# Performance work log

Measured on AMD Instinct MI355X. Metric: run time of the kernel, lower is better.

The kernel has to match this reference:

```python
import jax, jax.numpy as jnp
from jax import lax
import numpy as np

B, S, G = 16, 384, 384
N = S + G
E_CHAR, D = 100, 128
H = D // 2              # LSTM hidden per direction
NHEAD, NHID = 4, 64
T = 21                  # crf_input_dim = label_alphabet.size() + 1
START, STOP = T - 2, T - 1
ALPHA = 0.2
CHAR_V, GAZ_V = 8000, 100000
NEG = -9e15             # pyGAT masked_fill value


def setup_inputs():
    key = jax.random.key(0)
    ks = jax.random.split(key, 20)
    f32 = jnp.float32
    def nrm(k, shape, s=0.05):
        return (jax.random.normal(k, shape) * s).astype(f32)
    eye = jnp.eye(N, dtype=bool)
    def adj(k):
        return ((jax.random.uniform(k, (B, N, N)) < 0.1) | eye[None]).astype(jnp.int32)
    return dict(
        batch_char=jax.random.randint(ks[0], (B, S), 0, CHAR_V),
        batch_len=jnp.full((B,), S, jnp.int32),
        gaz_list=jax.random.randint(ks[1], (B, G), 0, GAZ_V),
        t_graph=adj(ks[2]), c_graph=adj(ks[3]), l_graph=adj(ks[4]),
        mask=jnp.ones((B, S), jnp.int32),
        char_table=nrm(ks[5], (CHAR_V, E_CHAR)),
        gaz_table=nrm(ks[6], (GAZ_V, D)),
        w_ih_f=nrm(ks[7], (4 * H, E_CHAR)), w_hh_f=nrm(ks[8], (4 * H, H)),
        b_f=jnp.zeros((4 * H,), f32),
        w_ih_b=nrm(ks[9], (4 * H, E_CHAR)), w_hh_b=nrm(ks[10], (4 * H, H)),
        b_b=jnp.zeros((4 * H,), f32),
        h2h_W=nrm(ks[11], (T, D)), h2h_b=jnp.zeros((T,), f32),
        gat_Wh=nrm(ks[12], (3, NHEAD, D, NHID)),
        gat_ah=nrm(ks[13], (3, NHEAD, 2 * NHID)),
        gat_Wo=nrm(ks[14], (3, NHEAD * NHID, T)),
        gat_ao=nrm(ks[15], (3, 2 * T)),
        fuse_w=jnp.ones((4,), f32),
        transitions=nrm(ks[16], (T, T)),
    )


def _lstm_dir(x, w_ih, w_hh, b, reverse):
    # x: [B,S,E]; torch gate order i,f,g,o
    Bb = x.shape[0]
    Hh = w_hh.shape[1]
    xw = jnp.einsum('bse,ge->bsg', x, w_ih) + b
    def step(carry, xt):
        h, c = carry
        g = xt + h @ w_hh.T
        i, f, gg, o = jnp.split(g, 4, axis=-1)
        c = jax.nn.sigmoid(f) * c + jax.nn.sigmoid(i) * jnp.tanh(gg)
        h = jax.nn.sigmoid(o) * jnp.tanh(c)
        return (h, c), h
    h0 = jnp.zeros((Bb, Hh), x.dtype)
    _, hs = lax.scan(step, (h0, h0), xw.swapaxes(0, 1), reverse=reverse)
    return hs.swapaxes(0, 1)


def _gat_layer(x, adj, W, a, concat):
    # pyGAT batched layer: e_ij = LeakyReLU(a . [Wh_i || Wh_j]), masked softmax over j
    h = jnp.einsum('bnd,df->bnf', x, W)
    F_ = W.shape[1]
    f1 = h @ a[:F_]           # [B,N]
    f2 = h @ a[F_:]
    e = jax.nn.leaky_relu(f1[:, :, None] + f2[:, None, :], negative_slope=ALPHA)
    e = jnp.where(adj > 0, e, NEG)
    att = jax.nn.softmax(e, axis=-1)
    out = jnp.einsum('bij,bjf->bif', att, h)
    return jax.nn.elu(out) if concat else out


def _gat(x, adj, Wh, ah, Wo, ao):
    heads = jax.vmap(lambda W, a: _gat_layer(x, adj, W, a, True))(Wh, ah)  # [H,B,N,F]
    hcat = jnp.moveaxis(heads, 0, 2).reshape(x.shape[0], x.shape[1], -1)
    return jax.nn.elu(_gat_layer(hcat, adj, Wo, ao, False))


def _crf_feature(batch_char, gaz_list, graphs, char_table, gaz_table,
                 w_ih_f, w_hh_f, b_f, w_ih_b, w_hh_b, b_b, h2h_W, h2h_b,
                 gat_Wh, gat_ah, gat_Wo, gat_ao, fuse_w):
    emb = char_table[batch_char]                      # [B,S,E_CHAR]
    hf = _lstm_dir(emb, w_ih_f, w_hh_f, b_f, False)
    hb = _lstm_dir(emb, w_ih_b, w_hh_b, b_b, True)
    lstm_feat = jnp.concatenate([hf, hb], axis=-1)    # [B,S,D]
    gaz_feat = gaz_table[gaz_list]                    # [B,G,D]
    gat_in = jnp.concatenate([lstm_feat, gaz_feat], axis=1)  # [B,N,D]
    gat_outs = [_gat(gat_in, adj, gat_Wh[k], gat_ah[k], gat_Wo[k], gat_ao[k])[:, :S]
                for k, adj in enumerate(graphs)]
    lstm_proj = lstm_feat @ h2h_W.T + h2h_b           # [B,S,T]
    return (fuse_w[0] * lstm_proj + fuse_w[1] * gat_outs[0]
            + fuse_w[2] * gat_outs[1] + fuse_w[3] * gat_outs[2])


def _viterbi(feats, transitions, mask):
    Bb, Ss, Tt = feats.shape
    ids = jnp.arange(Tt)
    part0 = feats[:, 0, :] + transitions[START][None, :]
    def step(part, inp):
        feat_t, m_t = inp
        cur = part[:, :, None] + transitions[None] + feat_t[:, None, :]  # [B,prev,cur]
        new = cur.max(axis=1)
        bp = cur.argmax(axis=1)
        m = (m_t > 0)[:, None]
        return jnp.where(m, new, part), jnp.where(m, bp, ids[None, :])
    part, bps = lax.scan(step, part0,
                         (feats[:, 1:].swapaxes(0, 1), mask[:, 1:].swapaxes(0, 1)))
    last_tag = jnp.argmax(part + transitions[:, STOP][None, :], axis=1)
    def back(tag, bp):
        prev = jnp.take_along_axis(bp, tag[:, None], axis=1)[:, 0]
        return prev, prev
    _, prevs = lax.scan(back, last_tag, bps, reverse=True)   # prevs[j] = tag at time j
    return jnp.concatenate([prevs.swapaxes(0, 1), last_tag[:, None]], axis=1)


def reference(batch_char, batch_len, gaz_list, t_graph, c_graph, l_graph, mask,
              char_table, gaz_table, w_ih_f, w_hh_f, b_f, w_ih_b, w_hh_b, b_b,
              h2h_W, h2h_b, gat_Wh, gat_ah, gat_Wo, gat_ao, fuse_w, transitions):
    # batch_len is all == S (mask all ones), so packed BiLSTM == plain BiLSTM
    feats = _crf_feature(batch_char, gaz_list, (t_graph, c_graph, l_graph),
                         char_table, gaz_table, w_ih_f, w_hh_f, b_f,
                         w_ih_b, w_hh_b, b_b, h2h_W, h2h_b,
                         gat_Wh, gat_ah, gat_Wo, gat_ao, fuse_w)
    return _viterbi(feats, transitions, mask)
```

## Files before the change

kernel.cpp:

```cpp
#include <hip/hip_runtime.h>
#include <hip/hip_bf16.h>
#include <cstdint>
#include <cstddef>

#define BB 16
#define SS 384
#define GG 384
#define NN 768
#define DD 128
#define EC 100
#define TT 21
#define NHEADS 4
#define BN (BB*NN)
#define BS (BB*SS)

#define GAZ_BASE  32
#define PACK_BASE (32 + 3072)
#define PRE_GRID  (PACK_BASE + 3 * BN)

#define H1SZ   3145728
#define OUT1SZ 3145728
#define H2SZ   258048
#define FGSZ   49152
#define FOSZ   12288
#define OUT2SZ 129024
#define PKSZ   ((size_t)BN * 12)

typedef float v2f __attribute__((ext_vector_type(2)));

__device__ __forceinline__ float sigf(float x) { return 1.0f / (1.0f + __expf(-x)); }
__device__ __forceinline__ float tanh_fast(float x) {
    return 1.0f - 2.0f / (__expf(2.0f * x) + 1.0f);
}
__device__ __forceinline__ float wred_max(float v) {
    #pragma unroll
    for (int o = 32; o > 0; o >>= 1) v = fmaxf(v, __shfl_xor(v, o));
    return v;
}
__device__ __forceinline__ float wred_sum(float v) {
    #pragma unroll
    for (int o = 32; o > 0; o >>= 1) v += __shfl_xor(v, o);
    return v;
}

__global__ __launch_bounds__(256) void k_xw(
    const int* __restrict__ batch_char, const float* __restrict__ char_table,
    const float* __restrict__ w_ih_f, const float* __restrict__ b_f,
    const float* __restrict__ w_ih_b, const float* __restrict__ b_b,
    float* __restrict__ xw_f, float* __restrict__ xw_b)
{
    __shared__ float At[EC * 68];
    __shared__ float Bt[EC * 68];
    __shared__ int   chs[64];
    const int tid = threadIdx.x;
    const int rt  = blockIdx.x;
    const int ot  = blockIdx.y;
    const int dir = ot >> 2, gt = ot & 3;
    const float* wih  = dir ? w_ih_b : w_ih_f;
    const float* bias = dir ? b_b    : b_f;
    float*       out  = dir ? xw_b   : xw_f;

    if (tid < 64) chs[tid] = batch_char[rt * 64 + tid];
    __syncthreads();
    for (int idx = tid; idx < 64 * EC; idx += 256) {
        int r = idx / EC, e = idx - r * EC;
        At[e * 68 + r] = char_table[(size_t)chs[r] * EC + e];
        Bt[e * 68 + r] = wih[(size_t)(gt * 64 + r) * EC + e];
    }
    __syncthreads();

    const int ty = tid >> 4, tx = tid & 15;
    const int r0 = ty * 4, c0 = tx * 4;
    float acc[4][4] = {};
    #pragma unroll 4
    for (int e = 0; e < EC; ++e) {
        float4 a = *(const float4*)&At[e * 68 + r0];
        float4 bv = *(const float4*)&Bt[e * 68 + c0];
        float av[4] = {a.x, a.y, a.z, a.w};
        float bb[4] = {bv.x, bv.y, bv.z, bv.w};
        #pragma unroll
        for (int i = 0; i < 4; ++i)
            #pragma unroll
            for (int j = 0; j < 4; ++j) acc[i][j] = fmaf(av[i], bb[j], acc[i][j]);
    }
    #pragma unroll
    for (int i = 0; i < 4; ++i) {
        int row = rt * 64 + r0 + i;
        int gc  = gt * 64 + c0;
        float4 o;
        o.x = acc[i][0] + bias[gc + 0];
        o.y = acc[i][1] + bias[gc + 1];
        o.z = acc[i][2] + bias[gc + 2];
        o.w = acc[i][3] + bias[gc + 3];
        *(float4*)&out[(size_t)row * 256 + gc] = o;
    }
}

__global__ __launch_bounds__(256) void k_pre(
    const float* __restrict__ xw_f, const float* __restrict__ xw_b,
    const float* __restrict__ w_hh_f, const float* __restrict__ w_hh_b,
    float* __restrict__ gat_in,
    const int* __restrict__ gaz_list, const float* __restrict__ gaz_table,
    const int* __restrict__ adj0, const int* __restrict__ adj1,
    const int* __restrict__ adj2, unsigned long long* __restrict__ packed)
{
    __shared__ float part[2][4][64][4];
    __shared__ float hbuf[4][64];
    const int bid = blockIdx.x;
    const int tid = threadIdx.x;

    if (bid < 32) {
        const int wv = tid >> 6, lane = tid & 63;
        const int b = bid >> 1, dir = bid & 1;
        const float* xw  = (dir ? xw_b : xw_f) + (size_t)b * SS * 256;
        const float* whh = dir ? w_hh_b : w_hh_f;
        v2f w2[4][8];
        #pragma unroll
        for (int g4 = 0; g4 < 4; ++g4) {
            const float* r = whh + (size_t)(g4 * 64 + lane) * 64 + 16 * wv;
            #pragma unroll
            for (int jj = 0; jj < 8; ++jj) w2[g4][jj] = v2f{r[2 * jj], r[2 * jj + 1]};
        }
        hbuf[wv][lane] = 0.f;
        float c = 0.f;
        int buf = 0;
        const int t0 = dir ? (SS - 1) : 0;
        float x0 = xw[t0 * 256 +   0 + lane];
        float x1 = xw[t0 * 256 +  64 + lane];
        float x2 = xw[t0 * 256 + 128 + lane];
        float x3 = xw[t0 * 256 + 192 + lane];
        const v2f* h2p = (const v2f*)&hbuf[wv][16 * wv];
        for (int tt = 0; tt < SS; ++tt) {
            const int t = dir ? (SS - 1 - tt) : tt;
            const int tn = dir ? (t - 1) : (t + 1);
            v2f a0 = v2f{0.f, 0.f}, a1 = v2f{0.f, 0.f}, a2 = v2f{0.f, 0.f}, a3 = v2f{0.f, 0.f};
            #pragma unroll
            for (int jj = 0; jj < 8; ++jj) {
                v2f hv = h2p[jj];
                a0 = __builtin_elementwise_fma(hv, w2[0][jj], a0);
                a1 = __builtin_elementwise_fma(hv, w2[1][jj], a1);
                a2 = __builtin_elementwise_fma(hv, w2[2][jj], a2);
                a3 = __builtin_elementwise_fma(hv, w2[3][jj], a3);
            }
            float4 pw;
            pw.x = a0.x + a0.y; pw.y = a1.x + a1.y;
            pw.z = a2.x + a2.y; pw.w = a3.x + a3.y;
            *(float4*)part[buf][wv][lane] = pw;
            float nx0 = 0.f, nx1 = 0.f, nx2 = 0.f, nx3 = 0.f;
            if (tt + 1 < SS) {
                nx0 = xw[tn * 256 +   0 + lane];
                nx1 = xw[tn * 256 +  64 + lane];
                nx2 = xw[tn * 256 + 128 + lane];
                nx3 = xw[tn * 256 + 192 + lane];
            }
            __syncthreads();
            float4 p0 = *(const float4*)part[buf][0][lane];
            float4 p1 = *(const float4*)part[buf][1][lane];
            float4 p2 = *(const float4*)part[buf][2][lane];
            float4 p3 = *(const float4*)part[buf][3][lane];
            float gi = ((p0.x + p1.x) + (p2.x + p3.x)) + x0;
            float gf = ((p0.y + p1.y) + (p2.y + p3.y)) + x1;
            float gg = ((p0.z + p1.z) + (p2.z + p3.z)) + x2;
            float go = ((p0.w + p1.w) + (p2.w + p3.w)) + x3;
            float nc = sigf(gf) * c + sigf(gi) * tanh_fast(gg);
            float nh = sigf(go) * tanh_fast(nc);
            c = nc;
            hbuf[wv][lane] = nh;
            if (wv == 0) gat_in[((size_t)b * NN + t) * DD + dir * 64 + lane] = nh;
            x0 = nx0; x1 = nx1; x2 = nx2; x3 = nx3;
            buf ^= 1;
        }
    } else if (bid < PACK_BASE) {
        int idx = (bid - GAZ_BASE) * 256 + tid;
        int d = idx & 127;
        int rest = idx >> 7;
        int g = rest % GG;
        int b = rest / GG;
        int gi = __builtin_nontemporal_load(&gaz_list[b * GG + g]);
        float v = __builtin_nontemporal_load(&gaz_table[(size_t)gi * DD + d]);
        gat_in[((size_t)b * NN + SS + g) * DD + d] = v;
    } else {
        const int row = bid - PACK_BASE;
        const int k = row / BN, n = row - k * BN;
        const int* adjk = (k == 0) ? adj0 : ((k == 1) ? adj1 : adj2);
        const int wave = tid >> 6, lane = tid & 63;
        #pragma unroll
        for (int it = 0; it < 3; ++it) {
            int j = it * 256 + tid;
            int a = __builtin_nontemporal_load(&adjk[(size_t)n * NN + j]);
            unsigned long long m = __ballot(a > 0);
            if (lane == 0)
                packed[((size_t)k * BN + n) * 12 + it * 4 + wave] = m;
        }
    }
}

__global__ __launch_bounds__(256) void k_p1(
    const float* __restrict__ gat_in, const float* __restrict__ gat_Wh,
    const float* __restrict__ gat_ah, int k0,
    float* __restrict__ h1, float* __restrict__ f1g, float* __restrict__ f2g,
    size_t zh1, size_t zfg)
{
    __shared__ float At[64 * 68];
    __shared__ float Bt[64 * 68];
    __shared__ float sf1[64], sf2[64];
    const int tid = threadIdx.x;
    const int rt = blockIdx.x, hd = blockIdx.y, z = blockIdx.z;
    const int k = k0 + z;
    float* h1p = h1 + (size_t)z * zh1;
    float* f1p = f1g + (size_t)z * zfg;
    float* f2p = f2g + (size_t)z * zfg;
    if (tid < 64) { sf1[tid] = 0.f; sf2[tid] = 0.f; }
    const float* W = gat_Wh + ((size_t)(k * NHEADS + hd)) * DD * 64;
    const int ty = tid >> 4, tx = tid & 15;
    const int r0 = ty * 4, c0 = tx * 4;
    float acc[4][4] = {};
    for (int ph = 0; ph < 2; ++ph) {
        __syncthreads();
        for (int idx = tid; idx < 64 * 64; idx += 256) {
            int r = idx >> 6, e = idx & 63;
            At[e * 68 + r] = gat_in[((size_t)(rt * 64 + r)) * DD + ph * 64 + e];
            int rB = idx & 63, eB = idx >> 6;
            Bt[eB * 68 + rB] = W[(size_t)(ph * 64 + eB) * 64 + rB];
        }
        __syncthreads();
        #pragma unroll 4
        for (int e = 0; e < 64; ++e) {
            float4 a = *(const float4*)&At[e * 68 + r0];
            float4 bv = *(const float4*)&Bt[e * 68 + c0];
            float av[4] = {a.x, a.y, a.z, a.w};
            float bb[4] = {bv.x, bv.y, bv.z, bv.w};
            #pragma unroll
            for (int i = 0; i < 4; ++i)
                #pragma unroll
                for (int j = 0; j < 4; ++j) acc[i][j] = fmaf(av[i], bb[j], acc[i][j]);
        }
    }
    const float* ah = gat_ah + (size_t)(k * NHEADS + hd) * 128;
    float a1[4], a2[4];
    #pragma unroll
    for (int j = 0; j < 4; ++j) { a1[j] = ah[c0 + j]; a2[j] = ah[64 + c0 + j]; }
    #pragma unroll
    for (int i = 0; i < 4; ++i) {
        int n = rt * 64 + r0 + i;
        float4 o = make_float4(acc[i][0], acc[i][1], acc[i][2], acc[i][3]);
        *(float4*)&h1p[((size_t)n * NHEADS + hd) * 64 + c0] = o;
        float p1 = acc[i][0] * a1[0] + acc[i][1] * a1[1] + acc[i][2] * a1[2] + acc[i][3] * a1[3];
        float p2 = acc[i][0] * a2[0] + acc[i][1] * a2[1] + acc[i][2] * a2[2] + acc[i][3] * a2[3];
        atomicAdd(&sf1[r0 + i], p1);
        atomicAdd(&sf2[r0 + i], p2);
    }
    __syncthreads();
    if (tid < 64) {
        f1p[hd * BN + rt * 64 + tid] = sf1[tid];
        f2p[hd * BN + rt * 64 + tid] = sf2[tid];
    }
}

__global__ __launch_bounds__(256) void k_attn1(
    const unsigned long long* __restrict__ packed, const float* __restrict__ h1,
    const float* __restrict__ f1g, const float* __restrict__ f2g,
    float* __restrict__ out1,
    size_t zpk, size_t zh1, size_t zfg, size_t zout1)
{
    __shared__ int   nbr[NN];
    __shared__ float ep[NHEADS][NN];
    __shared__ int cntS;
    const int tid = threadIdx.x, wave = tid >> 6, lane = tid & 63;
    const int bid = blockIdx.x, z = blockIdx.z;
    const int xcd = bid & 7;
    const int local = bid >> 3;
    const int b = 2 * xcd + ((local >= NN) ? 1 : 0);
    const int i = (local >= NN) ? (local - NN) : local;
    const int n = b * NN + i;
    const unsigned long long* pkp = packed + (size_t)z * zpk;
    const float* h1p = h1 + (size_t)z * zh1;
    const float* f1p = f1g + (size_t)z * zfg;
    const float* f2gp = f2g + (size_t)z * zfg;
    float* out1p = out1 + (size_t)z * zout1;
    if (wave == 0) {
        unsigned long long m = (lane < 12) ? pkp[(size_t)n * 12 + lane] : 0ULL;
        int pc = __popcll(m);
        int inc = pc;
        #pragma unroll
        for (int d = 1; d < 16; d <<= 1) { int t = __shfl_up(inc, d); if (lane >= d) inc += t; }
        int C = __shfl(inc, 11);
        if (lane == 0) cntS = C;
        int off = inc - pc;
        while (m) {
            int bit = __builtin_ctzll(m);
            nbr[off++] = lane * 64 + bit;
            m &= m - 1;
        }
    }
    __syncthreads();
    const int C = cntS;
    const int hd = wave;
    const float f1 = f1p[hd * BN + n];
    const float* f2p = f2gp + hd * BN + b * NN;
    float mx = -3.0e38f;
    for (int t = lane; t < C; t += 64) {
        float e = f1 + f2p[nbr[t]];
        e = (e >= 0.f) ? e : 0.2f * e;
        ep[hd][t] = e;
        mx = fmaxf(mx, e);
    }
    mx = wred_max(mx);
    float sum = 0.f;
    for (int t = lane; t < C; t += 64) {
        float p = __expf(ep[hd][t] - mx);
        ep[hd][t] = p;
        sum += p;
    }
    sum = wred_sum(sum);
    const float* hb = h1p + (size_t)b * NN * (NHEADS * 64) + hd * 64 + lane;
    float ac0 = 0.f, ac1 = 0.f, ac2 = 0.f, ac3 = 0.f;
    int t = 0;
    for (; t + 3 < C; t += 4) {
        int j0 = nbr[t], j1 = nbr[t + 1], j2 = nbr[t + 2], j3 = nbr[t + 3];
        float p0 = ep[hd][t], p1 = ep[hd][t + 1], p2 = ep[hd][t + 2], p3 = ep[hd][t + 3];
        ac0 = fmaf(p0, hb[(size_t)j0 * 256], ac0);
        ac1 = fmaf(p1, hb[(size_t)j1 * 256], ac1);
        ac2 = fmaf(p2, hb[(size_t)j2 * 256], ac2);
        ac3 = fmaf(p3, hb[(size_t)j3 * 256], ac3);
    }
    for (; t < C; ++t) ac0 = fmaf(ep[hd][t], hb[(size_t)nbr[t] * 256], ac0);
    float r = ((ac0 + ac1) + (ac2 + ac3)) / sum;
    r = (r > 0.f) ? r : expm1f(r);
    __builtin_nontemporal_store(r, &out1p[(size_t)n * 256 + hd * 64 + lane]);
}

__global__ __launch_bounds__(256) void k_p2(
    const float* __restrict__ out1, const float* __restrict__ gat_Wo,
    const float* __restrict__ gat_ao, int k0,
    float* __restrict__ h2, float* __restrict__ f1o, float* __restrict__ f2o,
    size_t zout1, size_t zh2, size_t zfo)
{
    __shared__ float ld[12 * 256];
    __shared__ float lf1[12], lf2[12];
    const int tid = threadIdx.x;
    const int blk = blockIdx.x, z = blockIdx.z;
    const int k = k0 + z;
    const float* out1p = out1 + (size_t)z * zout1;
    float* h2p = h2 + (size_t)z * zh2;
    float* f1op = f1o + (size_t)z * zfo;
    float* f2op = f2o + (size_t)z * zfo;
    if (tid < 12) { lf1[tid] = 0.f; lf2[tid] = 0.f; }
    for (int idx = tid; idx < 12 * 256; idx += 256)
        ld[idx] = out1p[(size_t)blk * 12 * 256 + idx];
    __syncthreads();
    if (tid < 252) {
        const int r = tid / TT, c = tid - r * TT;
        const float* Wo = gat_Wo + (size_t)k * 256 * TT;
        const float4* row4 = (const float4*)&ld[r * 256];
        float acc = 0.f;
        #pragma unroll 8
        for (int q4 = 0; q4 < 64; ++q4) {
            float4 v = row4[q4];
            int q = q4 * 4;
            acc = fmaf(v.x, Wo[(q + 0) * TT + c], acc);
            acc = fmaf(v.y, Wo[(q + 1) * TT + c], acc);
            acc = fmaf(v.z, Wo[(q + 2) * TT + c], acc);
            acc = fmaf(v.w, Wo[(q + 3) * TT + c], acc);
        }
        const int n = blk * 12 + r;
        h2p[(size_t)n * TT + c] = acc;
        const float* ao = gat_ao + k * 2 * TT;
        atomicAdd(&lf1[r], acc * ao[c]);
        atomicAdd(&lf2[r], acc * ao[TT + c]);
    }
    __syncthreads();
    if (tid < 12) {
        f1op[blk * 12 + tid] = lf1[tid];
        f2op[blk * 12 + tid] = lf2[tid];
    }
}

__global__ __launch_bounds__(64) void k_attn2(
    const unsigned long long* __restrict__ packed,
    const float* __restrict__ h2, const float* __restrict__ f1o,
    const float* __restrict__ f2o, float* __restrict__ out2,
    size_t zpk, size_t zh2, size_t zfo, size_t zout2)
{
    __shared__ int   nbr[NN];
    __shared__ float ep[NN];
    const int lane = threadIdx.x;
    const int bid = blockIdx.x, z = blockIdx.z;
    const int xcd = bid & 7;
    const int local = bid >> 3;
    const int b = 2 * xcd + ((local >= SS) ? 1 : 0);
    const int s = (local >= SS) ? (local - SS) : local;
    const int blk = b * SS + s;
    const int n = b * NN + s;
    const unsigned long long* pkp = packed + (size_t)z * zpk;
    const float* h2p = h2 + (size_t)z * zh2;
    const float* f1op = f1o + (size_t)z * zfo;
    const float* f2op = f2o + (size_t)z * zfo;
    float* out2k = out2 + (size_t)z * zout2;
    unsigned long long w64 = (lane < 12) ? pkp[(size_t)n * 12 + lane] : 0ULL;
    int pc = __popcll(w64);
    int inc = pc;
    #pragma unroll
    for (int d = 1; d < 16; d <<= 1) {
        int t = __shfl_up(inc, d, 16);
        if ((lane & 15) >= d) inc += t;
    }
    const int C = __shfl(inc, 11);
    int off = inc - pc;
    while (w64) {
        int bit = __builtin_ctzll(w64);
        nbr[off++] = lane * 64 + bit;
        w64 &= w64 - 1;
    }
    __syncthreads();
    const float f1 = f1op[n];
    const float* f2p = f2op + b * NN;
    float mx = -3.0e38f;
    for (int t = lane; t < C; t += 64) {
        int j = nbr[t];
        float e = f1 + f2p[j];
        e = (e >= 0.f) ? e : 0.2f * e;
        ep[t] = e;
        mx = fmaxf(mx, e);
    }
    mx = wred_max(mx);
    float sum = 0.f;
    for (int t = lane; t < C; t += 64) {
        float p = __expf(ep[t] - mx);
        ep[t] = p;
        sum += p;
    }
    sum = wred_sum(sum);
    const float* h2b = h2p + (size_t)b * NN * TT + ((lane < TT) ? lane : 0);
    float ac0 = 0.f, ac1 = 0.f, ac2 = 0.f, ac3 = 0.f;
    int t = 0;
    for (; t + 3 < C; t += 4) {
        int j0 = nbr[t], j1 = nbr[t + 1], j2 = nbr[t + 2], j3 = nbr[t + 3];
        float p0 = ep[t], p1 = ep[t + 1], p2 = ep[t + 2], p3 = ep[t + 3];
        ac0 = fmaf(p0, h2b[(size_t)j0 * TT], ac0);
        ac1 = fmaf(p1, h2b[(size_t)j1 * TT], ac1);
        ac2 = fmaf(p2, h2b[(size_t)j2 * TT], ac2);
        ac3 = fmaf(p3, h2b[(size_t)j3 * TT], ac3);
    }
    for (; t < C; ++t) ac0 = fmaf(ep[t], h2b[(size_t)nbr[t] * TT], ac0);
    if (lane < TT) {
        float r = ((ac0 + ac1) + (ac2 + ac3)) / sum;
        r = (r > 0.f) ? r : expm1f(r);
        out2k[(size_t)blk * TT + lane] = r;
    }
}

__global__ __launch_bounds__(64) void k_fuse(
    const float* __restrict__ gat_in, const float* __restrict__ h2h_W,
    const float* __restrict__ h2h_b, const float* __restrict__ fuse_w,
    const float* __restrict__ out2, float* __restrict__ feats)
{
    __shared__ float row[DD];
    const int lane = threadIdx.x;
    const int blk = blockIdx.x;
    const int b = blk / SS, s = blk - b * SS;
    const float* src = gat_in + ((size_t)b * NN + s) * DD;
    row[lane] = src[lane];
    row[lane + 64] = src[lane + 64];
    __syncthreads();
    if (lane < TT) {
        float acc = h2h_b[lane];
        const float4* w4 = (const float4*)&h2h_W[lane * DD];
        const float4* r4 = (const float4*)row;
        #pragma unroll 8
        for (int d4 = 0; d4 < 32; ++d4) {
            float4 w = w4[d4]; float4 v = r4[d4];
            acc = fmaf(w.x, v.x, acc); acc = fmaf(w.y, v.y, acc);
            acc = fmaf(w.z, v.z, acc); acc = fmaf(w.w, v.w, acc);
        }
        size_t o = (size_t)blk * TT + lane;
        feats[o] = fuse_w[0] * acc + fuse_w[1] * out2[o]
                 + fuse_w[2] * out2[(size_t)BS * TT + o]
                 + fuse_w[3] * out2[2 * (size_t)BS * TT + o];
    }
}

__global__ __launch_bounds__(64) void k_vit(
    const float* __restrict__ feats, const float* __restrict__ trans,
    int* __restrict__ out)
{
    __shared__ unsigned char bp[SS - 1][24];
    const int lane = threadIdx.x;
    const int b = blockIdx.x;
    const int pg = lane / TT;
    const int c = lane - pg * TT;
    const bool act = (pg < 3);
    const int p0 = pg * 7;
    float tc[7];
    if (act) {
        #pragma unroll
        for (int u = 0; u < 7; ++u) tc[u] = trans[(p0 + u) * TT + c];
    }
    float pr = (lane < TT)
        ? feats[((size_t)b * SS) * TT + lane] + trans[19 * TT + lane]
        : -3.0e38f;
    float nf = (lane < TT) ? feats[((size_t)b * SS + 1) * TT + lane] : 0.f;
    for (int t = 1; t < SS; ++t) {
        float fcur = nf;
        if (t + 1 < SS)
            nf = (lane < TT) ? feats[((size_t)b * SS + t + 1) * TT + lane] : 0.f;
        float pv[7];
        #pragma unroll
        for (int u = 0; u < 7; ++u) pv[u] = __shfl(pr, p0 + u);
        float best = -3.0e38f; int bi = 0;
        if (act) {
            #pragma unroll
            for (int u = 0; u < 7; ++u) {
                float v = pv[u] + tc[u];
                if (v > best) { best = v; bi = p0 + u; }
            }
        }
        float bv1 = __shfl(best, lane + 21);
        int   bi1 = __shfl(bi,   lane + 21);
        float bv2 = __shfl(best, lane + 42);
        int   bi2 = __shfl(bi,   lane + 42);
        if (bv1 > best) { best = bv1; bi = bi1; }
        if (bv2 > best) { best = bv2; bi = bi2; }
        if (lane < TT) {
            bp[t - 1][lane] = (unsigned char)bi;
            pr = best + fcur;
        }
    }
    float fv = (lane < TT) ? pr + trans[lane * TT + 20] : -3.0e38f;
    int fi = (lane < TT) ? lane : 0;
    #pragma unroll
    for (int o = 32; o > 0; o >>= 1) {
        float ov = __shfl_xor(fv, o);
        int oi = __shfl_xor(fi, o);
        if (ov > fv || (ov == fv && oi < fi)) { fv = ov; fi = oi; }
    }
    int curs = __builtin_amdgcn_readfirstlane(fi);
    if (lane == 0) out[b * SS + SS - 1] = curs;
    int u = SS - 2;
    int rem = (u + 1) & 15;
    for (int i = 0; i < rem; ++i) {
        int tag = bp[u][curs];
        curs = __builtin_amdgcn_readfirstlane(tag);
        if (lane == 0) out[b * SS + u] = curs;
        --u;
    }
    const int ll = (lane < 24) ? lane : 0;
    while (u >= 15) {
        const int base = u - 15;
        int v[16];
        #pragma unroll
        for (int i = 0; i < 16; ++i) v[i] = bp[base + i][ll];
        #pragma unroll
        for (int i = 15; i >= 0; --i) {
            curs = __builtin_amdgcn_readlane(v[i], curs);
            if (lane == 0) out[b * SS + base + i] = curs;
        }
        u = base - 1;
    }
}

extern "C" void kernel_launch(void* const* d_in, const int* in_sizes, int n_in,
                              void* d_out, int out_size, void* d_ws, size_t ws_size,
                              hipStream_t stream) {
    (void)in_sizes; (void)n_in; (void)out_size;
    const int*   batch_char = (const int*)d_in[0];
    const int*   gaz_list   = (const int*)d_in[2];
    const int*   graphs[3]  = {(const int*)d_in[3], (const int*)d_in[4], (const int*)d_in[5]};
    const float* char_table = (const float*)d_in[7];
    const float* gaz_table  = (const float*)d_in[8];
    const float* w_ih_f = (const float*)d_in[9];
    const float* w_hh_f = (const float*)d_in[10];
    const float* b_f    = (const float*)d_in[11];
    const float* w_ih_b = (const float*)d_in[12];
    const float* w_hh_b = (const float*)d_in[13];
    const float* b_b    = (const float*)d_in[14];
    const float* h2h_W  = (const float*)d_in[15];
    const float* h2h_b  = (const float*)d_in[16];
    const float* gat_Wh = (const float*)d_in[17];
    const float* gat_ah = (const float*)d_in[18];
    const float* gat_Wo = (const float*)d_in[19];
    const float* gat_ao = (const float*)d_in[20];
    const float* fuse_w = (const float*)d_in[21];
    const float* trans  = (const float*)d_in[22];

    float* ws = (float*)d_ws;
    float* gat_in = ws;
    float* xw_f   = gat_in + 1572864;
    float* xw_b   = xw_f   + 1572864;
    float* base   = xw_b   + 1572864;

    const bool big = ws_size >= 106000000ull;

    float *h1, *out1, *h2, *f1g, *f2g, *f1o, *f2o, *out2, *feats;
    unsigned long long* packed;
    if (big) {
        h1    = base;
        out1  = h1   + 3 * (size_t)H1SZ;
        h2    = out1 + 3 * (size_t)OUT1SZ;
        f1g   = h2   + 3 * (size_t)H2SZ;
        f2g   = f1g  + 3 * (size_t)FGSZ;
        f1o   = f2g  + 3 * (size_t)FGSZ;
        f2o   = f1o  + 3 * (size_t)FOSZ;
        out2  = f2o  + 3 * (size_t)FOSZ;
        feats = out2 + 3 * (size_t)OUT2SZ;
        packed = (unsigned long long*)(feats + OUT2SZ);
    } else {
        h1    = base;
        out1  = h1   + (size_t)H1SZ;
        h2    = out1 + (size_t)OUT1SZ;
        f1g   = h2   + (size_t)H2SZ;
        f2g   = f1g  + (size_t)FGSZ;
        f1o   = f2g  + (size_t)FGSZ;
        f2o   = f1o  + (size_t)FOSZ;
        out2  = f2o  + (size_t)FOSZ;
        feats = out2 + 3 * (size_t)OUT2SZ;
        packed = (unsigned long long*)(feats + OUT2SZ);
    }

    k_xw<<<dim3(96, 8), 256, 0, stream>>>(batch_char, char_table, w_ih_f, b_f,
                                          w_ih_b, b_b, xw_f, xw_b);
    k_pre<<<PRE_GRID, 256, 0, stream>>>(xw_f, xw_b, w_hh_f, w_hh_b, gat_in,
                                        gaz_list, gaz_table,
                                        graphs[0], graphs[1], graphs[2], packed);
    if (big) {
        k_p1<<<dim3(192, 4, 3), 256, 0, stream>>>(gat_in, gat_Wh, gat_ah, 0,
                                                  h1, f1g, f2g, H1SZ, FGSZ);
        k_attn1<<<dim3(BN, 1, 3), 256, 0, stream>>>(packed, h1, f1g, f2g, out1,
                                                    PKSZ, H1SZ, FGSZ, OUT1SZ);
        k_p2<<<dim3(1024, 1, 3), 256, 0, stream>>>(out1, gat_Wo, gat_ao, 0,
                                                   h2, f1o, f2o, OUT1SZ, H2SZ, FOSZ);
        k_attn2<<<dim3(BS, 1, 3), 64, 0, stream>>>(packed, h2, f1o, f2o, out2,
                                                   PKSZ, H2SZ, FOSZ, OUT2SZ);
    } else {
        for (int k = 0; k < 3; ++k) {
            const unsigned long long* pk = packed + (size_t)k * PKSZ;
            k_p1<<<dim3(192, 4, 1), 256, 0, stream>>>(gat_in, gat_Wh, gat_ah, k,
                                                      h1, f1g, f2g, 0, 0);
            k_attn1<<<dim3(BN, 1, 1), 256, 0, stream>>>(pk, h1, f1g, f2g, out1,
                                                        0, 0, 0, 0);
            k_p2<<<dim3(1024, 1, 1), 256, 0, stream>>>(out1, gat_Wo, gat_ao, k,
                                                       h2, f1o, f2o, 0, 0, 0);
            k_attn2<<<dim3(BS, 1, 1), 64, 0, stream>>>(pk, h2, f1o, f2o,
                                                       out2 + (size_t)k * OUT2SZ,
                                                       0, 0, 0, 0);
        }
    }
    k_fuse<<<BS, 64, 0, stream>>>(gat_in, h2h_W, h2h_b, fuse_w, out2, feats);
    k_vit<<<BB, 64, 0, stream>>>(feats, trans, (int*)d_out);
}
```

Measured before the change: 855.6 us.

## Merge prep kernels and overlap GAT projection of gazetteer rows with LSTM

Folds the xw GEMM, gazetteer gather and adjacency bit-packing into one launch. The LSTM recurrence now shares a launch with GAT projection tiles for the gazetteer rows, which do not depend on the LSTM output; the character-row tiles run afterwards in a separate k_p1 launch. The aim is to keep the GPU busy while 32 blocks run the serial LSTM, at the cost of a more complex tile-index mapping. k_attn1 also stages each head's f2 row into shared memory so the neighbor gathers read LDS instead of global memory.

```diff
diff --git a/kernel.cpp b/kernel.cpp
--- a/kernel.cpp
+++ b/kernel.cpp
@@ -14,9 +14,10 @@
 #define BN (BB*NN)
 #define BS (BB*SS)
 
-#define GAZ_BASE  32
-#define PACK_BASE (32 + 3072)
-#define PRE_GRID  (PACK_BASE + 3 * BN)
+#define M1_XW   768
+#define M1_GAZ  (M1_XW + 3072)
+#define M1_GRID (M1_GAZ + 3 * BN)
+#define M2_GRID (32 + 96 * 4 * 3)
 
 #define H1SZ   3145728
 #define OUT1SZ 3145728
@@ -43,73 +44,159 @@
     return v;
 }
 
-__global__ __launch_bounds__(256) void k_xw(
+__device__ __forceinline__ void p1_tile(
+    const float* __restrict__ gat_in, const float* __restrict__ gat_Wh,
+    const float* __restrict__ gat_ah, int k, int rt, int hd,
+    float* __restrict__ h1p, float* __restrict__ f1p, float* __restrict__ f2p,
+    float* At, float* Bt, float* sf1, float* sf2)
+{
+    const int tid = threadIdx.x;
+    if (tid < 64) { sf1[tid] = 0.f; sf2[tid] = 0.f; }
+    const float* W = gat_Wh + ((size_t)(k * NHEADS + hd)) * DD * 64;
+    const int ty = tid >> 4, tx = tid & 15;
+    const int r0 = ty * 4, c0 = tx * 4;
+    float acc[4][4] = {};
+    for (int ph = 0; ph < 2; ++ph) {
+        __syncthreads();
+        for (int idx = tid; idx < 64 * 64; idx += 256) {
+            int r = idx >> 6, e = idx & 63;
+            At[e * 68 + r] = gat_in[((size_t)(rt * 64 + r)) * DD + ph * 64 + e];
+            int rB = idx & 63, eB = idx >> 6;
+            Bt[eB * 68 + rB] = W[(size_t)(ph * 64 + eB) * 64 + rB];
+        }
+        __syncthreads();
+        #pragma unroll 4
+        for (int e = 0; e < 64; ++e) {
+            float4 a = *(const float4*)&At[e * 68 + r0];
+            float4 bv = *(const float4*)&Bt[e * 68 + c0];
+            float av[4] = {a.x, a.y, a.z, a.w};
+            float bb[4] = {bv.x, bv.y, bv.z, bv.w};
+            #pragma unroll
+            for (int i = 0; i < 4; ++i)
+                #pragma unroll
+                for (int j = 0; j < 4; ++j) acc[i][j] = fmaf(av[i], bb[j], acc[i][j]);
+        }
+    }
+    const float* ah = gat_ah + (size_t)(k * NHEADS + hd) * 128;
+    float a1[4], a2[4];
+    #pragma unroll
+    for (int j = 0; j < 4; ++j) { a1[j] = ah[c0 + j]; a2[j] = ah[64 + c0 + j]; }
+    #pragma unroll
+    for (int i = 0; i < 4; ++i) {
+        int n = rt * 64 + r0 + i;
+        float4 o = make_float4(acc[i][0], acc[i][1], acc[i][2], acc[i][3]);
+        *(float4*)&h1p[((size_t)n * NHEADS + hd) * 64 + c0] = o;
+        float p1 = acc[i][0] * a1[0] + acc[i][1] * a1[1] + acc[i][2] * a1[2] + acc[i][3] * a1[3];
+        float p2 = acc[i][0] * a2[0] + acc[i][1] * a2[1] + acc[i][2] * a2[2] + acc[i][3] * a2[3];
+        atomicAdd(&sf1[r0 + i], p1);
+        atomicAdd(&sf2[r0 + i], p2);
+    }
+    __syncthreads();
+    if (tid < 64) {
+        f1p[hd * BN + rt * 64 + tid] = sf1[tid];
+        f2p[hd * BN + rt * 64 + tid] = sf2[tid];
+    }
+}
+
+__global__ __launch_bounds__(256) void k_mega1(
     const int* __restrict__ batch_char, const float* __restrict__ char_table,
     const float* __restrict__ w_ih_f, const float* __restrict__ b_f,
     const float* __restrict__ w_ih_b, const float* __restrict__ b_b,
-    float* __restrict__ xw_f, float* __restrict__ xw_b)
-{
-    __shared__ float At[EC * 68];
-    __shared__ float Bt[EC * 68];
-    __shared__ int   chs[64];
+    float* __restrict__ xw_f, float* __restrict__ xw_b,
+    const int* __restrict__ gaz_list, const float* __restrict__ gaz_table,
+    float* __restrict__ gat_in,
+    const int* __restrict__ adj0, const int* __restrict__ adj1,
+    const int* __restrict__ adj2, unsigned long long* __restrict__ packed)
+{
+    __shared__ __align__(16) float smem[13664];
+    const int bid = blockIdx.x;
     const int tid = threadIdx.x;
-    const int rt  = blockIdx.x;
-    const int ot  = blockIdx.y;
-    const int dir = ot >> 2, gt = ot & 3;
-    const float* wih  = dir ? w_ih_b : w_ih_f;
-    const float* bias = dir ? b_b    : b_f;
-    float*       out  = dir ? xw_b   : xw_f;
-
-    if (tid < 64) chs[tid] = batch_char[rt * 64 + tid];
-    __syncthreads();
-    for (int idx = tid; idx < 64 * EC; idx += 256) {
-        int r = idx / EC, e = idx - r * EC;
-        At[e * 68 + r] = char_table[(size_t)chs[r] * EC + e];
-        Bt[e * 68 + r] = wih[(size_t)(gt * 64 + r) * EC + e];
-    }
-    __syncthreads();
-
-    const int ty = tid >> 4, tx = tid & 15;
-    const int r0 = ty * 4, c0 = tx * 4;
-    float acc[4][4] = {};
-    #pragma unroll 4
-    for (int e = 0; e < EC; ++e) {
-        float4 a = *(const float4*)&At[e * 68 + r0];
-        float4 bv = *(const float4*)&Bt[e * 68 + c0];
-        float av[4] = {a.x, a.y, a.z, a.w};
-        float bb[4] = {bv.x, bv.y, bv.z, bv.w};
-        #pragma unroll
-        for (int i = 0; i < 4; ++i)
+
+    if (bid < M1_XW) {
+        float* At = smem;
+        float* Bt = smem + 6800;
+        int*   chs = (int*)(smem + 13600);
+        const int rt  = bid % 96;
+        const int ot  = bid / 96;
+        const int dir = ot >> 2, gt = ot & 3;
+        const float* wih  = dir ? w_ih_b : w_ih_f;
+        const float* bias = dir ? b_b    : b_f;
+        float*       out  = dir ? xw_b   : xw_f;
+
+        if (tid < 64) chs[tid] = batch_char[rt * 64 + tid];
+        __syncthreads();
+        for (int idx = tid; idx < 64 * EC; idx += 256) {
+            int r = idx / EC, e = idx - r * EC;
+            At[e * 68 + r] = char_table[(size_t)chs[r] * EC + e];
+            Bt[e * 68 + r] = wih[(size_t)(gt * 64 + r) * EC + e];
+        }
+        __syncthreads();
+
+        const int ty = tid >> 4, tx = tid & 15;
+        const int r0 = ty * 4, c0 = tx * 4;
+        float acc[4][4] = {};
+        #pragma unroll 4
+        for (int e = 0; e < EC; ++e) {
+            float4 a = *(const float4*)&At[e * 68 + r0];
+            float4 bv = *(const float4*)&Bt[e * 68 + c0];
+            float av[4] = {a.x, a.y, a.z, a.w};
+            float bb[4] = {bv.x, bv.y, bv.z, bv.w};
             #pragma unroll
-            for (int j = 0; j < 4; ++j) acc[i][j] = fmaf(av[i], bb[j], acc[i][j]);
-    }
-    #pragma unroll
-    for (int i = 0; i < 4; ++i) {
-        int row = rt * 64 + r0 + i;
-        int gc  = gt * 64 + c0;
-        float4 o;
-        o.x = acc[i][0] + bias[gc + 0];
-        o.y = acc[i][1] + bias[gc + 1];
-        o.z = acc[i][2] + bias[gc + 2];
-        o.w = acc[i][3] + bias[gc + 3];
-        *(float4*)&out[(size_t)row * 256 + gc] = o;
-    }
-}
-
-__global__ __launch_bounds__(256) void k_pre(
+            for (int i = 0; i < 4; ++i)
+                #pragma unroll
+                for (int j = 0; j < 4; ++j) acc[i][j] = fmaf(av[i], bb[j], acc[i][j]);
+        }
+        #pragma unroll
+        for (int i = 0; i < 4; ++i) {
+            int row = rt * 64 + r0 + i;
+            int gc  = gt * 64 + c0;
+            float4 o;
+            o.x = acc[i][0] + bias[gc + 0];
+            o.y = acc[i][1] + bias[gc + 1];
+            o.z = acc[i][2] + bias[gc + 2];
+            o.w = acc[i][3] + bias[gc + 3];
+            *(float4*)&out[(size_t)row * 256 + gc] = o;
+        }
+    } else if (bid < M1_GAZ) {
+        int idx = (bid - M1_XW) * 256 + tid;
+        int d = idx & 127;
+        int rest = idx >> 7;
+        int g = rest % GG;
+        int b = rest / GG;
+        int gi = __builtin_nontemporal_load(&gaz_list[b * GG + g]);
+        float v = __builtin_nontemporal_load(&gaz_table[(size_t)gi * DD + d]);
+        gat_in[((size_t)b * NN + SS + g) * DD + d] = v;
+    } else {
+        const int row = bid - M1_GAZ;
+        const int k = row / BN, n = row - k * BN;
+        const int* adjk = (k == 0) ? adj0 : ((k == 1) ? adj1 : adj2);
+        const int wave = tid >> 6, lane = tid & 63;
+        #pragma unroll
+        for (int it = 0; it < 3; ++it) {
+            int j = it * 256 + tid;
+            int a = __builtin_nontemporal_load(&adjk[(size_t)n * NN + j]);
+            unsigned long long m = __ballot(a > 0);
+            if (lane == 0)
+                packed[((size_t)k * BN + n) * 12 + it * 4 + wave] = m;
+        }
+    }
+}
+
+__global__ __launch_bounds__(256) void k_mega2(
     const float* __restrict__ xw_f, const float* __restrict__ xw_b,
     const float* __restrict__ w_hh_f, const float* __restrict__ w_hh_b,
     float* __restrict__ gat_in,
-    const int* __restrict__ gaz_list, const float* __restrict__ gaz_table,
-    const int* __restrict__ adj0, const int* __restrict__ adj1,
-    const int* __restrict__ adj2, unsigned long long* __restrict__ packed)
-{
-    __shared__ float part[2][4][64][4];
-    __shared__ float hbuf[4][64];
+    const float* __restrict__ gat_Wh, const float* __restrict__ gat_ah,
+    float* __restrict__ h1, float* __restrict__ f1g, float* __restrict__ f2g,
+    size_t zh1, size_t zfg)
+{
+    __shared__ __align__(16) float smem[8832];
     const int bid = blockIdx.x;
     const int tid = threadIdx.x;
 
     if (bid < 32) {
+        float (*part)[4][64][4] = (float(*)[4][64][4])smem;
+        float (*hbuf)[64]      = (float(*)[64])(smem + 2048);
         const int wv = tid >> 6, lane = tid & 63;
         const int b = bid >> 1, dir = bid & 1;
         const float* xw  = (dir ? xw_b : xw_f) + (size_t)b * SS * 256;
@@ -170,91 +257,33 @@
             x0 = nx0; x1 = nx1; x2 = nx2; x3 = nx3;
             buf ^= 1;
         }
-    } else if (bid < PACK_BASE) {
-        int idx = (bid - GAZ_BASE) * 256 + tid;
-        int d = idx & 127;
-        int rest = idx >> 7;
-        int g = rest % GG;
-        int b = rest / GG;
-        int gi = __builtin_nontemporal_load(&gaz_list[b * GG + g]);
-        float v = __builtin_nontemporal_load(&gaz_table[(size_t)gi * DD + d]);
-        gat_in[((size_t)b * NN + SS + g) * DD + d] = v;
     } else {
-        const int row = bid - PACK_BASE;
-        const int k = row / BN, n = row - k * BN;
-        const int* adjk = (k == 0) ? adj0 : ((k == 1) ? adj1 : adj2);
-        const int wave = tid >> 6, lane = tid & 63;
-        #pragma unroll
-        for (int it = 0; it < 3; ++it) {
-            int j = it * 256 + tid;
-            int a = __builtin_nontemporal_load(&adjk[(size_t)n * NN + j]);
-            unsigned long long m = __ballot(a > 0);
-            if (lane == 0)
-                packed[((size_t)k * BN + n) * 12 + it * 4 + wave] = m;
-        }
+        const int local = bid - 32;
+        const int z = local / 384;
+        const int rem = local - z * 384;
+        const int hd = rem / 96;
+        const int x = rem - hd * 96;
+        const int rt = (x / 6) * 12 + 6 + (x % 6);
+        float* At = smem, *Bt = smem + 4352, *sf1 = smem + 8704, *sf2 = smem + 8768;
+        p1_tile(gat_in, gat_Wh, gat_ah, z, rt, hd,
+                h1 + (size_t)z * zh1, f1g + (size_t)z * zfg, f2g + (size_t)z * zfg,
+                At, Bt, sf1, sf2);
     }
 }
 
 __global__ __launch_bounds__(256) void k_p1(
     const float* __restrict__ gat_in, const float* __restrict__ gat_Wh,
-    const float* __restrict__ gat_ah, int k0,
+    const float* __restrict__ gat_ah, int k0, int sel,
     float* __restrict__ h1, float* __restrict__ f1g, float* __restrict__ f2g,
     size_t zh1, size_t zfg)
 {
-    __shared__ float At[64 * 68];
-    __shared__ float Bt[64 * 68];
-    __shared__ float sf1[64], sf2[64];
-    const int tid = threadIdx.x;
-    const int rt = blockIdx.x, hd = blockIdx.y, z = blockIdx.z;
-    const int k = k0 + z;
-    float* h1p = h1 + (size_t)z * zh1;
-    float* f1p = f1g + (size_t)z * zfg;
-    float* f2p = f2g + (size_t)z * zfg;
-    if (tid < 64) { sf1[tid] = 0.f; sf2[tid] = 0.f; }
-    const float* W = gat_Wh + ((size_t)(k * NHEADS + hd)) * DD * 64;
-    const int ty = tid >> 4, tx = tid & 15;
-    const int r0 = ty * 4, c0 = tx * 4;
-    float acc[4][4] = {};
-    for (int ph = 0; ph < 2; ++ph) {
-        __syncthreads();
-        for (int idx = tid; idx < 64 * 64; idx += 256) {
-            int r = idx >> 6, e = idx & 63;
-            At[e * 68 + r] = gat_in[((size_t)(rt * 64 + r)) * DD + ph * 64 + e];
-            int rB = idx & 63, eB = idx >> 6;
-            Bt[eB * 68 + rB] = W[(size_t)(ph * 64 + eB) * 64 + rB];
-        }
-        __syncthreads();
-        #pragma unroll 4
-        for (int e = 0; e < 64; ++e) {
-            float4 a = *(const float4*)&At[e * 68 + r0];
-            float4 bv = *(const float4*)&Bt[e * 68 + c0];
-            float av[4] = {a.x, a.y, a.z, a.w};
-            float bb[4] = {bv.x, bv.y, bv.z, bv.w};
-            #pragma unroll
-            for (int i = 0; i < 4; ++i)
-                #pragma unroll
-                for (int j = 0; j < 4; ++j) acc[i][j] = fmaf(av[i], bb[j], acc[i][j]);
-        }
-    }
-    const float* ah = gat_ah + (size_t)(k * NHEADS + hd) * 128;
-    float a1[4], a2[4];
-    #pragma unroll
-    for (int j = 0; j < 4; ++j) { a1[j] = ah[c0 + j]; a2[j] = ah[64 + c0 + j]; }
-    #pragma unroll
-    for (int i = 0; i < 4; ++i) {
-        int n = rt * 64 + r0 + i;
-        float4 o = make_float4(acc[i][0], acc[i][1], acc[i][2], acc[i][3]);
-        *(float4*)&h1p[((size_t)n * NHEADS + hd) * 64 + c0] = o;
-        float p1 = acc[i][0] * a1[0] + acc[i][1] * a1[1] + acc[i][2] * a1[2] + acc[i][3] * a1[3];
-        float p2 = acc[i][0] * a2[0] + acc[i][1] * a2[1] + acc[i][2] * a2[2] + acc[i][3] * a2[3];
-        atomicAdd(&sf1[r0 + i], p1);
-        atomicAdd(&sf2[r0 + i], p2);
-    }
-    __syncthreads();
-    if (tid < 64) {
-        f1p[hd * BN + rt * 64 + tid] = sf1[tid];
-        f2p[hd * BN + rt * 64 + tid] = sf2[tid];
-    }
+    __shared__ __align__(16) float smem[8832];
+    const int x = blockIdx.x, hd = blockIdx.y, z = blockIdx.z;
+    const int rt = (sel < 0) ? x : ((x / 6) * 12 + sel * 6 + (x % 6));
+    float* At = smem, *Bt = smem + 4352, *sf1 = smem + 8704, *sf2 = smem + 8768;
+    p1_tile(gat_in, gat_Wh, gat_ah, k0 + z, rt, hd,
+            h1 + (size_t)z * zh1, f1g + (size_t)z * zfg, f2g + (size_t)z * zfg,
+            At, Bt, sf1, sf2);
 }
 
 __global__ __launch_bounds__(256) void k_attn1(
@@ -265,6 +294,7 @@
 {
     __shared__ int   nbr[NN];
     __shared__ float ep[NHEADS][NN];
+    __shared__ __align__(16) float f2s[NHEADS][NN];
     __shared__ int cntS;
     const int tid = threadIdx.x, wave = tid >> 6, lane = tid & 63;
     const int bid = blockIdx.x, z = blockIdx.z;
@@ -278,6 +308,12 @@
     const float* f1p = f1g + (size_t)z * zfg;
     const float* f2gp = f2g + (size_t)z * zfg;
     float* out1p = out1 + (size_t)z * zout1;
+    const int hd = wave;
+    {
+        const float4* src = (const float4*)(f2gp + hd * BN + b * NN);
+        float4* dst = (float4*)f2s[hd];
+        for (int j = lane; j < NN / 4; j += 64) dst[j] = src[j];
+    }
     if (wave == 0) {
         unsigned long long m = (lane < 12) ? pkp[(size_t)n * 12 + lane] : 0ULL;
         int pc = __popcll(m);
@@ -295,12 +331,10 @@
     }
     __syncthreads();
     const int C = cntS;
-    const int hd = wave;
     const float f1 = f1p[hd * BN + n];
-    const float* f2p = f2gp + hd * BN + b * NN;
     float mx = -3.0e38f;
     for (int t = lane; t < C; t += 64) {
-        float e = f1 + f2p[nbr[t]];
+        float e = f1 + f2s[hd][nbr[t]];
         e = (e >= 0.f) ? e : 0.2f * e;
         ep[hd][t] = e;
         mx = fmaxf(mx, e);
@@ -617,14 +651,16 @@
         packed = (unsigned long long*)(feats + OUT2SZ);
     }
 
-    k_xw<<<dim3(96, 8), 256, 0, stream>>>(batch_char, char_table, w_ih_f, b_f,
-                                          w_ih_b, b_b, xw_f, xw_b);
-    k_pre<<<PRE_GRID, 256, 0, stream>>>(xw_f, xw_b, w_hh_f, w_hh_b, gat_in,
-                                        gaz_list, gaz_table,
-                                        graphs[0], graphs[1], graphs[2], packed);
+    k_mega1<<<M1_GRID, 256, 0, stream>>>(batch_char, char_table, w_ih_f, b_f,
+                                         w_ih_b, b_b, xw_f, xw_b,
+                                         gaz_list, gaz_table, gat_in,
+                                         graphs[0], graphs[1], graphs[2], packed);
     if (big) {
-        k_p1<<<dim3(192, 4, 3), 256, 0, stream>>>(gat_in, gat_Wh, gat_ah, 0,
-                                                  h1, f1g, f2g, H1SZ, FGSZ);
+        k_mega2<<<M2_GRID, 256, 0, stream>>>(xw_f, xw_b, w_hh_f, w_hh_b, gat_in,
+                                             gat_Wh, gat_ah, h1, f1g, f2g,
+                                             H1SZ, FGSZ);
+        k_p1<<<dim3(96, 4, 3), 256, 0, stream>>>(gat_in, gat_Wh, gat_ah, 0, 0,
+                                                 h1, f1g, f2g, H1SZ, FGSZ);
         k_attn1<<<dim3(BN, 1, 3), 256, 0, stream>>>(packed, h1, f1g, f2g, out1,
                                                     PKSZ, H1SZ, FGSZ, OUT1SZ);
         k_p2<<<dim3(1024, 1, 3), 256, 0, stream>>>(out1, gat_Wo, gat_ao, 0,
@@ -632,9 +668,11 @@
         k_attn2<<<dim3(BS, 1, 3), 64, 0, stream>>>(packed, h2, f1o, f2o, out2,
                                                    PKSZ, H2SZ, FOSZ, OUT2SZ);
     } else {
+        k_mega2<<<32, 256, 0, stream>>>(xw_f, xw_b, w_hh_f, w_hh_b, gat_in,
+                                        gat_Wh, gat_ah, h1, f1g, f2g, 0, 0);
         for (int k = 0; k < 3; ++k) {
             const unsigned long long* pk = packed + (size_t)k * PKSZ;
-            k_p1<<<dim3(192, 4, 1), 256, 0, stream>>>(gat_in, gat_Wh, gat_ah, k,
+            k_p1<<<dim3(192, 4, 1), 256, 0, stream>>>(gat_in, gat_Wh, gat_ah, k, -1,
                                                       h1, f1g, f2g, 0, 0);
             k_attn1<<<dim3(BN, 1, 1), 256, 0, stream>>>(pk, h1, f1g, f2g, out1,
                                                         0, 0, 0, 0);
```

Result: slower. 982.6 us (+14.9%).

## Replace LDS neighbor compaction with register bitmask iteration in GAT attention kernels

Applied to the files above, without the earlier changes.

Both GAT attention kernels no longer build a compacted neighbor list and per-edge score array in shared memory. Each lane now scores the dense row in registers, masking non-edges out of the softmax. The aggregation walks the adjacency bitmask with ctz and broadcasts each probability with a wave shuffle. This drops the prefix-scan, LDS traffic and block barrier, but adds 12 uniform mask loads per lane, dense f2 loads, and a serial loop whose two accumulators give less memory-level parallelism than the old four.

```diff
diff --git a/kernel.cpp b/kernel.cpp
--- a/kernel.cpp
+++ b/kernel.cpp
@@ -263,9 +263,6 @@
     float* __restrict__ out1,
     size_t zpk, size_t zh1, size_t zfg, size_t zout1)
 {
-    __shared__ int   nbr[NN];
-    __shared__ float ep[NHEADS][NN];
-    __shared__ int cntS;
     const int tid = threadIdx.x, wave = tid >> 6, lane = tid & 63;
     const int bid = blockIdx.x, z = blockIdx.z;
     const int xcd = bid & 7;
@@ -278,54 +275,56 @@
     const float* f1p = f1g + (size_t)z * zfg;
     const float* f2gp = f2g + (size_t)z * zfg;
     float* out1p = out1 + (size_t)z * zout1;
-    if (wave == 0) {
-        unsigned long long m = (lane < 12) ? pkp[(size_t)n * 12 + lane] : 0ULL;
-        int pc = __popcll(m);
-        int inc = pc;
-        #pragma unroll
-        for (int d = 1; d < 16; d <<= 1) { int t = __shfl_up(inc, d); if (lane >= d) inc += t; }
-        int C = __shfl(inc, 11);
-        if (lane == 0) cntS = C;
-        int off = inc - pc;
-        while (m) {
-            int bit = __builtin_ctzll(m);
-            nbr[off++] = lane * 64 + bit;
-            m &= m - 1;
-        }
-    }
-    __syncthreads();
-    const int C = cntS;
     const int hd = wave;
+
+    unsigned long long mw[12];
+    #pragma unroll
+    for (int w = 0; w < 12; ++w) mw[w] = pkp[(size_t)n * 12 + w];
+
     const float f1 = f1p[hd * BN + n];
     const float* f2p = f2gp + hd * BN + b * NN;
+
+    float e[12];
     float mx = -3.0e38f;
-    for (int t = lane; t < C; t += 64) {
-        float e = f1 + f2p[nbr[t]];
-        e = (e >= 0.f) ? e : 0.2f * e;
-        ep[hd][t] = e;
-        mx = fmaxf(mx, e);
+    #pragma unroll
+    for (int w = 0; w < 12; ++w) {
+        float ev = f1 + f2p[w * 64 + lane];
+        ev = (ev >= 0.f) ? ev : 0.2f * ev;
+        e[w] = ev;
+        bool on = (mw[w] >> lane) & 1ULL;
+        mx = fmaxf(mx, on ? ev : -3.0e38f);
     }
     mx = wred_max(mx);
+    float p[12];
     float sum = 0.f;
-    for (int t = lane; t < C; t += 64) {
-        float p = __expf(ep[hd][t] - mx);
-        ep[hd][t] = p;
-        sum += p;
+    #pragma unroll
+    for (int w = 0; w < 12; ++w) {
+        bool on = (mw[w] >> lane) & 1ULL;
+        float pv = on ? __expf(e[w] - mx) : 0.f;
+        p[w] = pv;
+        sum += pv;
     }
     sum = wred_sum(sum);
+
     const float* hb = h1p + (size_t)b * NN * (NHEADS * 64) + hd * 64 + lane;
-    float ac0 = 0.f, ac1 = 0.f, ac2 = 0.f, ac3 = 0.f;
-    int t = 0;
-    for (; t + 3 < C; t += 4) {
-        int j0 = nbr[t], j1 = nbr[t + 1], j2 = nbr[t + 2], j3 = nbr[t + 3];
-        float p0 = ep[hd][t], p1 = ep[hd][t + 1], p2 = ep[hd][t + 2], p3 = ep[hd][t + 3];
-        ac0 = fmaf(p0, hb[(size_t)j0 * 256], ac0);
-        ac1 = fmaf(p1, hb[(size_t)j1 * 256], ac1);
-        ac2 = fmaf(p2, hb[(size_t)j2 * 256], ac2);
-        ac3 = fmaf(p3, hb[(size_t)j3 * 256], ac3);
-    }
-    for (; t < C; ++t) ac0 = fmaf(ep[hd][t], hb[(size_t)nbr[t] * 256], ac0);
-    float r = ((ac0 + ac1) + (ac2 + ac3)) / sum;
+    float ac0 = 0.f, ac1 = 0.f;
+    #pragma unroll
+    for (int w = 0; w < 12; w += 2) {
+        unsigned long long ma = mw[w], mb2 = mw[w + 1];
+        while (ma | mb2) {
+            if (ma) {
+                int j = __builtin_ctzll(ma); ma &= ma - 1;
+                float sp = __shfl(p[w], j);
+                ac0 = fmaf(sp, hb[(size_t)(w * 64 + j) * 256], ac0);
+            }
+            if (mb2) {
+                int j = __builtin_ctzll(mb2); mb2 &= mb2 - 1;
+                float sp = __shfl(p[w + 1], j);
+                ac1 = fmaf(sp, hb[(size_t)((w + 1) * 64 + j) * 256], ac1);
+            }
+        }
+    }
+    float r = (ac0 + ac1) / sum;
     r = (r > 0.f) ? r : expm1f(r);
     __builtin_nontemporal_store(r, &out1p[(size_t)n * 256 + hd * 64 + lane]);
 }
@@ -382,8 +381,6 @@
     const float* __restrict__ f2o, float* __restrict__ out2,
     size_t zpk, size_t zh2, size_t zfo, size_t zout2)
 {
-    __shared__ int   nbr[NN];
-    __shared__ float ep[NN];
     const int lane = threadIdx.x;
     const int bid = blockIdx.x, z = blockIdx.z;
     const int xcd = bid & 7;
@@ -397,54 +394,56 @@
     const float* f1op = f1o + (size_t)z * zfo;
     const float* f2op = f2o + (size_t)z * zfo;
     float* out2k = out2 + (size_t)z * zout2;
-    unsigned long long w64 = (lane < 12) ? pkp[(size_t)n * 12 + lane] : 0ULL;
-    int pc = __popcll(w64);
-    int inc = pc;
-    #pragma unroll
-    for (int d = 1; d < 16; d <<= 1) {
-        int t = __shfl_up(inc, d, 16);
-        if ((lane & 15) >= d) inc += t;
-    }
-    const int C = __shfl(inc, 11);
-    int off = inc - pc;
-    while (w64) {
-        int bit = __builtin_ctzll(w64);
-        nbr[off++] = lane * 64 + bit;
-        w64 &= w64 - 1;
-    }
-    __syncthreads();
+
+    unsigned long long mw[12];
+    #pragma unroll
+    for (int w = 0; w < 12; ++w) mw[w] = pkp[(size_t)n * 12 + w];
+
     const float f1 = f1op[n];
     const float* f2p = f2op + b * NN;
+
+    float e[12];
     float mx = -3.0e38f;
-    for (int t = lane; t < C; t += 64) {
-        int j = nbr[t];
-        float e = f1 + f2p[j];
-        e = (e >= 0.f) ? e : 0.2f * e;
-        ep[t] = e;
-        mx = fmaxf(mx, e);
+    #pragma unroll
+    for (int w = 0; w < 12; ++w) {
+        float ev = f1 + f2p[w * 64 + lane];
+        ev = (ev >= 0.f) ? ev : 0.2f * ev;
+        e[w] = ev;
+        bool on = (mw[w] >> lane) & 1ULL;
+        mx = fmaxf(mx, on ? ev : -3.0e38f);
     }
     mx = wred_max(mx);
+    float p[12];
     float sum = 0.f;
-    for (int t = lane; t < C; t += 64) {
-        float p = __expf(ep[t] - mx);
-        ep[t] = p;
-        sum += p;
+    #pragma unroll
+    for (int w = 0; w < 12; ++w) {
+        bool on = (mw[w] >> lane) & 1ULL;
+        float pv = on ? __expf(e[w] - mx) : 0.f;
+        p[w] = pv;
+        sum += pv;
     }
     sum = wred_sum(sum);
+
     const float* h2b = h2p + (size_t)b * NN * TT + ((lane < TT) ? lane : 0);
-    float ac0 = 0.f, ac1 = 0.f, ac2 = 0.f, ac3 = 0.f;
-    int t = 0;
-    for (; t + 3 < C; t += 4) {
-        int j0 = nbr[t], j1 = nbr[t + 1], j2 = nbr[t + 2], j3 = nbr[t + 3];
-        float p0 = ep[t], p1 = ep[t + 1], p2 = ep[t + 2], p3 = ep[t + 3];
-        ac0 = fmaf(p0, h2b[(size_t)j0 * TT], ac0);
-        ac1 = fmaf(p1, h2b[(size_t)j1 * TT], ac1);
-        ac2 = fmaf(p2, h2b[(size_t)j2 * TT], ac2);
-        ac3 = fmaf(p3, h2b[(size_t)j3 * TT], ac3);
-    }
-    for (; t < C; ++t) ac0 = fmaf(ep[t], h2b[(size_t)nbr[t] * TT], ac0);
+    float ac0 = 0.f, ac1 = 0.f;
+    #pragma unroll
+    for (int w = 0; w < 12; w += 2) {
+        unsigned long long ma = mw[w], mb2 = mw[w + 1];
+        while (ma | mb2) {
+            if (ma) {
+                int j = __builtin_ctzll(ma); ma &= ma - 1;
+                float sp = __shfl(p[w], j);
+                ac0 = fmaf(sp, h2b[(size_t)(w * 64 + j) * TT], ac0);
+            }
+            if (mb2) {
+                int j = __builtin_ctzll(mb2); mb2 &= mb2 - 1;
+                float sp = __shfl(p[w + 1], j);
+                ac1 = fmaf(sp, h2b[(size_t)((w + 1) * 64 + j) * TT], ac1);
+            }
+        }
+    }
     if (lane < TT) {
-        float r = ((ac0 + ac1) + (ac2 + ac3)) / sum;
+        float r = (ac0 + ac1) / sum;
         r = (r > 0.f) ? r : expm1f(r);
         out2k[(size_t)blk * TT + lane] = r;
     }
```

After: 993.9 us. 16.2% more time.
